# Kernel optimization log

Hardware: AMD Instinct MI355X
Metric: run time of the kernel (lower is better)

Reference implementation:

```python
import jax, jax.numpy as jnp
import numpy as np

B, N, C = 8, 1024, 768
H, D = 12, 64  # num_heads, head_dim; C == H*D
SCALE = 1.0 / np.sqrt(D)
NEG_INF = -1e9


def setup_inputs() -> dict:
    key = jax.random.key(0)
    k1, k2, k3, k4 = jax.random.split(key, 4)
    x = jax.random.normal(k1, (B, N, C), dtype=jnp.float32)
    # additive padding mask: 0 for valid tokens, -1e9 for padded tail
    lengths = jax.random.randint(k2, (B,), N // 2, N + 1)  # valid lengths per sample
    pad = jnp.arange(N)[None, :] >= lengths[:, None]       # [B, N] True = padded
    attn_mask = jnp.where(pad, NEG_INF, 0.0).astype(jnp.float32)[:, None, None, :]  # [B,1,1,N]
    W_qkv = jax.random.normal(k3, (C, 3 * C), dtype=jnp.float32) * (C ** -0.5)
    b_qkv = jnp.zeros((3 * C,), dtype=jnp.float32)
    W_proj = jax.random.normal(k4, (C, C), dtype=jnp.float32) * (C ** -0.5)
    b_proj = jnp.zeros((C,), dtype=jnp.float32)
    return {"x": x, "attn_mask": attn_mask, "W_qkv": W_qkv, "b_qkv": b_qkv,
            "W_proj": W_proj, "b_proj": b_proj}


def reference(x, attn_mask, W_qkv, b_qkv, W_proj, b_proj):
    qkv = (x @ W_qkv + b_qkv).reshape(B, N, 3, H, D)
    qkv = jnp.transpose(qkv, (2, 0, 3, 1, 4))
    q, k, v = qkv[0], qkv[1], qkv[2]
    attn = jnp.einsum('bhnd,bhmd->bhnm', q, k) * SCALE  # [B, H, N, N]
    attn = attn + attn_mask                              # broadcast [B,1,1,N]
    attn = jax.nn.softmax(attn, axis=-1)
    out = jnp.einsum('bhnm,bhmd->bhnd', attn, v)         # [B, H, N, D]
    out = jnp.transpose(out, (0, 2, 1, 3)).reshape(B, N, C)
    return out @ W_proj + b_proj
```

## Files before the change

kernel.cpp:

```cpp
#include <hip/hip_runtime.h>
#include <stdint.h>

#define NB 8
#define NHEAD 12
#define SEQ 1024
#define CDIM 768
#define HDIM 64

#define SCALE_L2E 0.1803368801111244f
#define L2E 1.4426950408889634f

typedef __attribute__((ext_vector_type(8))) short bf16x8;
typedef __attribute__((ext_vector_type(4))) short bf16x4;
typedef __attribute__((ext_vector_type(4))) float f32x4;
typedef __attribute__((ext_vector_type(4))) unsigned short us4;

__device__ __forceinline__ void gload_lds16(const void* g, void* l) {
  __builtin_amdgcn_global_load_lds((const __attribute__((address_space(1))) void*)g,
                                   (__attribute__((address_space(3))) void*)l,
                                   16, 0, 0);
}

__device__ __forceinline__ unsigned short f2bf(float f) {
  __bf16 h = (__bf16)f;
  return __builtin_bit_cast(unsigned short, h);
}

__device__ __forceinline__ f32x4 mfma16(bf16x8 a, bf16x8 b, f32x4 c) {
  return __builtin_amdgcn_mfma_f32_16x16x32_bf16(a, b, c, 0, 0, 0);
}


__global__ void cvt_x_kernel(const float* __restrict__ in,
                             unsigned short* __restrict__ out, int n8) {
  int i = blockIdx.x * blockDim.x + threadIdx.x;
  if (i >= n8) return;
  const float4* p = (const float4*)in;
  float4 a = p[2 * i], b = p[2 * i + 1];
  union { bf16x8 v; unsigned short h[8]; } u;
  u.h[0] = f2bf(a.x); u.h[1] = f2bf(a.y); u.h[2] = f2bf(a.z); u.h[3] = f2bf(a.w);
  u.h[4] = f2bf(b.x); u.h[5] = f2bf(b.y); u.h[6] = f2bf(b.z); u.h[7] = f2bf(b.w);
  ((bf16x8*)out)[i] = u.v;
}

__global__ void tconv_kernel(const float* __restrict__ in,
                             unsigned short* __restrict__ out, int K, int N) {
  __shared__ float tile[32][33];
  int tx = threadIdx.x & 31, ty = threadIdx.x >> 5;
  int n0 = blockIdx.x * 32, k0 = blockIdx.y * 32;
#pragma unroll
  for (int i = 0; i < 4; i++)
    tile[ty + 8 * i][tx] = in[(size_t)(k0 + ty + 8 * i) * N + n0 + tx];
  __syncthreads();
#pragma unroll
  for (int i = 0; i < 4; i++)
    out[(size_t)(n0 + ty + 8 * i) * K + k0 + tx] = f2bf(tile[tx][ty + 8 * i]);
}

template <int BM, int BN, int EPI>
__global__ __launch_bounds__(256, 4)
void gemm_bt_kernel(const unsigned short* __restrict__ A,
                    const unsigned short* __restrict__ Bt,
                    const float* __restrict__ bias,
                    unsigned short* __restrict__ q_out,
                    unsigned short* __restrict__ k_out,
                    unsigned short* __restrict__ v_out,
                    float* __restrict__ f_out,
                    int M, int N, int K) {
  constexpr int WM = BM / 2, WN = BN / 2;
  constexpr int MI = WM / 16, NJ = WN / 16;
  constexpr int CA = BM / 32, CB = BN / 32;
  __shared__ __align__(16) unsigned short As[BM * 64];
  __shared__ __align__(16) unsigned short Bs[BN * 64];
  const int t = threadIdx.x;
  const int w = t >> 6, l = t & 63;
  const int g = l >> 4, lr = l & 15;
  const int wr = w >> 1, wc = w & 1;
  const int nTN = N / BN;
  const int bpx = gridDim.x >> 3;
  const int orig = (blockIdx.x & 7) * bpx + (blockIdx.x >> 3);
  const int bm = orig / nTN, bn = orig % nTN;
  const int m0 = bm * BM, n0 = bn * BN;

  f32x4 acc[MI][NJ];
#pragma unroll
  for (int i = 0; i < MI; i++)
#pragma unroll
    for (int j = 0; j < NJ; j++) acc[i][j] = f32x4{0.f, 0.f, 0.f, 0.f};

  const unsigned short* aP[CA];
  const unsigned short* bP[CB];
#pragma unroll
  for (int i = 0; i < CA; i++) {
    int c = t + 256 * i, r = c >> 3, s = c & 7;
    aP[i] = A + (size_t)(m0 + r) * K + (s ^ (r & 7)) * 8;
  }
#pragma unroll
  for (int i = 0; i < CB; i++) {
    int c = t + 256 * i, r = c >> 3, s = c & 7;
    bP[i] = Bt + (size_t)(n0 + r) * K + (s ^ (r & 7)) * 8;
  }

  bf16x8 areg[CA], breg[CB];
  auto prefetch = [&](int kk) {
#pragma unroll
    for (int i = 0; i < CA; i++) areg[i] = *(const bf16x8*)(aP[i] + kk);
#pragma unroll
    for (int i = 0; i < CB; i++) breg[i] = *(const bf16x8*)(bP[i] + kk);
  };
  auto commit = [&]() {
#pragma unroll
    for (int i = 0; i < CA; i++) *(bf16x8*)(As + (t + 256 * i) * 8) = areg[i];
#pragma unroll
    for (int i = 0; i < CB; i++) *(bf16x8*)(Bs + (t + 256 * i) * 8) = breg[i];
  };

  prefetch(0);
  for (int kk = 0; kk < K; kk += 64) {
    commit();
    __syncthreads();
    if (kk + 64 < K) prefetch(kk + 64);
#pragma unroll
    for (int ks = 0; ks < 2; ks++) {
      const int slot = ((ks * 4 + g) ^ (lr & 7)) << 3;
      bf16x8 af[MI];
#pragma unroll
      for (int i = 0; i < MI; i++) {
        int row = wr * WM + i * 16 + lr;
        af[i] = *(const bf16x8*)(As + row * 64 + slot);
      }
#pragma unroll
      for (int j = 0; j < NJ; j++) {
        int row = wc * WN + j * 16 + lr;
        bf16x8 bfr = *(const bf16x8*)(Bs + row * 64 + slot);
#pragma unroll
        for (int i = 0; i < MI; i++) acc[i][j] = mfma16(af[i], bfr, acc[i][j]);
      }
    }
    __syncthreads();
  }

  float bv[NJ];
#pragma unroll
  for (int j = 0; j < NJ; j++) bv[j] = bias[n0 + wc * WN + j * 16 + lr];

  if (EPI == 1) {
#pragma unroll
    for (int i = 0; i < MI; i++) {
      int mrow = m0 + wr * WM + i * 16 + 4 * g;
#pragma unroll
      for (int j = 0; j < NJ; j++) {
        int n = n0 + wc * WN + j * 16 + lr;
#pragma unroll
        for (int r = 0; r < 4; r++)
          f_out[(size_t)(mrow + r) * N + n] = acc[i][j][r] + bv[j];
      }
    }
  } else {
    const int which = n0 / CDIM;
    const int bb = m0 / SEQ;
    const int tok0 = (m0 % SEQ) + wr * WM;
#pragma unroll
    for (int j = 0; j < NJ; j++) {
      int ncol = (n0 % CDIM) + wc * WN + j * 16;
      int hh = ncol / 64;
      int d = (ncol % 64) + lr;
#pragma unroll
      for (int i = 0; i < MI; i++) {
        int tokb = tok0 + i * 16 + 4 * g;
        if (which == 2) {
          us4 pk;
#pragma unroll
          for (int r = 0; r < 4; r++) pk[r] = f2bf(acc[i][j][r] + bv[j]);
          *(us4*)(v_out + ((size_t)(bb * NHEAD + hh) * 64 + d) * SEQ + tokb) = pk;
        } else {
          unsigned short* dst = (which == 0) ? q_out : k_out;
#pragma unroll
          for (int r = 0; r < 4; r++)
            dst[((size_t)(bb * NHEAD + hh) * SEQ + tokb + r) * 64 + d] =
                f2bf(acc[i][j][r] + bv[j]);
        }
      }
    }
  }
}

__global__ __launch_bounds__(256, 3)
void attn_kernel(const unsigned short* __restrict__ Qb,
                 const unsigned short* __restrict__ Kb,
                 const unsigned short* __restrict__ Vt,
                 const float* __restrict__ mask,
                 unsigned short* __restrict__ Ob) {
  __shared__ __align__(16) unsigned short Qs[128 * 64];
  __shared__ __align__(16) unsigned short Ks[128 * 64];
  __shared__ __align__(16) unsigned short Vs[64 * 128];
  __shared__ __align__(16) float smask[128];

  const int hwb = blockIdx.x;
  const int x = hwb & 7;
  const int i = hwb >> 3;
  const int qt = i & 7;
  const int bh = (i >> 3) * 8 + x;
  const int h = bh % NHEAD, b = bh / NHEAD;

  const int t = threadIdx.x, w = t >> 6, l = t & 63;
  const int g = l >> 4, lr = l & 15;

  const unsigned short* Qg = Qb + (((size_t)b * NHEAD + h) * SEQ + qt * 128) * 64;
  const unsigned short* Kg = Kb + ((size_t)b * NHEAD + h) * SEQ * 64;
  const unsigned short* Vg = Vt + ((size_t)b * NHEAD + h) * 64 * SEQ;
  const float* mg = mask + (size_t)b * SEQ;

  int nkb = 8;
#pragma unroll
  for (int kb = 7; kb >= 4; kb--)
    if (mg[kb * 128] < -1e8f) nkb = kb;

  bf16x8 kreg[4], vreg[4];
  float mreg;
  auto prefetch = [&](int kb) {
#pragma unroll
    for (int ii = 0; ii < 4; ii++) {
      int c = t + 256 * ii;
      int rk = c >> 3, sk = c & 7;
      kreg[ii] = *(const bf16x8*)(Kg + (size_t)(kb * 128 + rk) * 64 +
                                  ((sk ^ (rk & 7)) << 3));
      int rv = c >> 4, sv = c & 15;
      vreg[ii] = *(const bf16x8*)(Vg + (size_t)rv * SEQ + kb * 128 +
                                  ((sv ^ (rv & 7)) << 3));
    }
    mreg = (t < 128) ? mg[kb * 128 + t] * L2E : 0.f;
  };
  auto commit = [&]() {
#pragma unroll
    for (int ii = 0; ii < 4; ii++) {
      *(bf16x8*)(Ks + (t + 256 * ii) * 8) = kreg[ii];
      *(bf16x8*)(Vs + (t + 256 * ii) * 8) = vreg[ii];
    }
    if (t < 128) smask[t] = mreg;
  };

#pragma unroll
  for (int ii = 0; ii < 4; ii++) {
    int c = t + 256 * ii;
    int row = c >> 3, sl = c & 7;
    gload_lds16(Qg + row * 64 + ((sl ^ (row & 7)) << 3), Qs + c * 8);
  }
  prefetch(0);
  __syncthreads();

  bf16x8 qfr[2][2];
#pragma unroll
  for (int qi = 0; qi < 2; qi++)
#pragma unroll
    for (int ks = 0; ks < 2; ks++) {
      int row = w * 32 + qi * 16 + lr;
      qfr[qi][ks] =
          *(const bf16x8*)(Qs + row * 64 + (((ks * 4 + g) ^ (lr & 7)) << 3));
    }

  float l_run[2] = {0.f, 0.f};
  f32x4 oacc[2][4];
#pragma unroll
  for (int qi = 0; qi < 2; qi++)
#pragma unroll
    for (int df = 0; df < 4; df++) oacc[qi][df] = f32x4{0.f, 0.f, 0.f, 0.f};

  for (int kb = 0; kb < nkb; kb++) {
    __syncthreads();
    commit();
    __syncthreads();
    if (kb + 1 < nkb) prefetch(kb + 1);

    float bs[2] = {0.f, 0.f};
    bf16x8 pa[4][2];
#pragma unroll
    for (int kc = 0; kc < 4; kc++) {
      f32x4 s0[2], s1[2];
#pragma unroll
      for (int qi = 0; qi < 2; qi++) {
        s0[qi] = f32x4{0.f, 0.f, 0.f, 0.f};
        s1[qi] = f32x4{0.f, 0.f, 0.f, 0.f};
      }
#pragma unroll
      for (int ks = 0; ks < 2; ks++) {
        int row0 = (2 * kc) * 16 + lr;
        int row1 = (2 * kc + 1) * 16 + lr;
        int slot = ((ks * 4 + g) ^ (lr & 7)) << 3;
        bf16x8 a0 = *(const bf16x8*)(Ks + row0 * 64 + slot);
        bf16x8 a1 = *(const bf16x8*)(Ks + row1 * 64 + slot);
        s0[0] = mfma16(a0, qfr[0][ks], s0[0]);
        s0[1] = mfma16(a0, qfr[1][ks], s0[1]);
        s1[0] = mfma16(a1, qfr[0][ks], s1[0]);
        s1[1] = mfma16(a1, qfr[1][ks], s1[1]);
      }
      f32x4 mv0 = *(const f32x4*)(smask + (2 * kc) * 16 + 4 * g);
      f32x4 mv1 = *(const f32x4*)(smask + (2 * kc + 1) * 16 + 4 * g);
#pragma unroll
      for (int qi = 0; qi < 2; qi++) {
        union { bf16x8 v; unsigned short hh[8]; } u;
#pragma unroll
        for (int r = 0; r < 4; r++) {
          float p0 = __builtin_amdgcn_exp2f(fmaf(s0[qi][r], SCALE_L2E, mv0[r]));
          float p1 = __builtin_amdgcn_exp2f(fmaf(s1[qi][r], SCALE_L2E, mv1[r]));
          bs[qi] += p0 + p1;
          u.hh[r] = f2bf(p0);
          u.hh[4 + r] = f2bf(p1);
        }
        pa[kc][qi] = u.v;
      }
    }
    bs[0] += __shfl_xor(bs[0], 16);
    bs[0] += __shfl_xor(bs[0], 32);
    bs[1] += __shfl_xor(bs[1], 16);
    bs[1] += __shfl_xor(bs[1], 32);
    l_run[0] += bs[0];
    l_run[1] += bs[1];

    const int sw = (lr & 7) << 4;
#pragma unroll
    for (int kc = 0; kc < 4; kc++) {
#pragma unroll
      for (int df = 0; df < 4; df++) {
        const char* vp = (const char*)(Vs + (df * 16 + lr) * 128);
        bf16x4 lo = *(const bf16x4*)(vp + ((kc * 64 + 8 * g) ^ sw));
        bf16x4 hi = *(const bf16x4*)(vp + ((kc * 64 + 32 + 8 * g) ^ sw));
        bf16x8 vb = __builtin_shufflevector(lo, hi, 0, 1, 2, 3, 4, 5, 6, 7);
        oacc[0][df] = mfma16(pa[kc][0], vb, oacc[0][df]);
        oacc[1][df] = mfma16(pa[kc][1], vb, oacc[1][df]);
      }
    }
  }

#pragma unroll
  for (int qi = 0; qi < 2; qi++) {
    float linv = 1.f / l_run[qi];
#pragma unroll
    for (int r = 0; r < 4; r++) {
      float li = __shfl(linv, 4 * g + r);
      int tok = qt * 128 + w * 32 + qi * 16 + 4 * g + r;
#pragma unroll
      for (int df = 0; df < 4; df++) {
        float val = oacc[qi][df][r] * li;
        Ob[((size_t)b * SEQ + tok) * CDIM + h * 64 + df * 16 + lr] = f2bf(val);
      }
    }
  }
}

extern "C" void kernel_launch(void* const* d_in, const int* in_sizes, int n_in,
                              void* d_out, int out_size, void* d_ws,
                              size_t ws_size, hipStream_t stream) {
  const float* x = (const float*)d_in[0];
  const float* mask = (const float*)d_in[1];
  const float* Wqkv = (const float*)d_in[2];
  const float* bqkv = (const float*)d_in[3];
  const float* Wproj = (const float*)d_in[4];
  const float* bproj = (const float*)d_in[5];
  float* out = (float*)d_out;

  char* ws = (char*)d_ws;
  size_t off = 0;
  auto take = [&](size_t bytes) {
    char* p = ws + off;
    off += (bytes + 255) & ~(size_t)255;
    return p;
  };
  unsigned short* xb = (unsigned short*)take((size_t)NB * SEQ * CDIM * 2);
  unsigned short* wqt = (unsigned short*)take((size_t)3 * CDIM * CDIM * 2);
  unsigned short* wpt = (unsigned short*)take((size_t)CDIM * CDIM * 2);
  unsigned short* Qb = (unsigned short*)take((size_t)NB * NHEAD * SEQ * 64 * 2);
  unsigned short* Kbf = (unsigned short*)take((size_t)NB * NHEAD * SEQ * 64 * 2);
  unsigned short* Vt = (unsigned short*)take((size_t)NB * NHEAD * SEQ * 64 * 2);
  unsigned short* Ob = (unsigned short*)take((size_t)NB * SEQ * CDIM * 2);

  int n8 = NB * SEQ * CDIM / 8;
  cvt_x_kernel<<<(n8 + 255) / 256, 256, 0, stream>>>(x, xb, n8);
  tconv_kernel<<<dim3(3 * CDIM / 32, CDIM / 32), 256, 0, stream>>>(Wqkv, wqt,
                                                                   CDIM, 3 * CDIM);
  tconv_kernel<<<dim3(CDIM / 32, CDIM / 32), 256, 0, stream>>>(Wproj, wpt, CDIM,
                                                               CDIM);
  gemm_bt_kernel<128, 128, 0>
      <<<(NB * SEQ / 128) * (3 * CDIM / 128), 256, 0, stream>>>(
          xb, wqt, bqkv, Qb, Kbf, Vt, nullptr, NB * SEQ, 3 * CDIM, CDIM);
  attn_kernel<<<NB * NHEAD * 8, 256, 0, stream>>>(Qb, Kbf, Vt, mask, Ob);
  gemm_bt_kernel<64, 64, 1>
      <<<(NB * SEQ / 64) * (CDIM / 64), 256, 0, stream>>>(
          Ob, wpt, bproj, nullptr, nullptr, nullptr, out, NB * SEQ, CDIM, CDIM);
}
```

Measured before the change: 214.9 us.

## Double-buffer GEMM tiles via direct global-to-LDS loads and widen V swizzle

The GEMM main loop switches from register-staged prefetch to global_load_lds writes straight into double-buffered shared tiles. Explicit vmcnt waits and raw barriers let the next tile's load overlap the current tile's MFMAs. The attention kernel's V tile swizzle grows from 8 to 16 chunk positions to cut LDS bank conflicts on the split 8-byte V reads. Doubling shared memory lowers the occupancy hint to 2 for the QKV GEMM variant, which may reduce latency hiding.

```diff
diff --git a/kernel.cpp b/kernel.cpp
--- a/kernel.cpp
+++ b/kernel.cpp
@@ -28,6 +28,14 @@
 
 __device__ __forceinline__ f32x4 mfma16(bf16x8 a, bf16x8 b, f32x4 c) {
   return __builtin_amdgcn_mfma_f32_16x16x32_bf16(a, b, c, 0, 0, 0);
+}
+
+template <int N>
+__device__ __forceinline__ void s_waitcnt_vm() {
+  if constexpr (N == 0) asm volatile("s_waitcnt vmcnt(0)" ::: "memory");
+  else if constexpr (N == 4) asm volatile("s_waitcnt vmcnt(4)" ::: "memory");
+  else if constexpr (N == 8) asm volatile("s_waitcnt vmcnt(8)" ::: "memory");
+  else static_assert(N == 0, "unsupported vmcnt literal");
 }
 
 
@@ -58,7 +66,7 @@
 }
 
 template <int BM, int BN, int EPI>
-__global__ __launch_bounds__(256, 4)
+__global__ __launch_bounds__(256, EPI ? 4 : 2)
 void gemm_bt_kernel(const unsigned short* __restrict__ A,
                     const unsigned short* __restrict__ Bt,
                     const float* __restrict__ bias,
@@ -70,8 +78,9 @@
   constexpr int WM = BM / 2, WN = BN / 2;
   constexpr int MI = WM / 16, NJ = WN / 16;
   constexpr int CA = BM / 32, CB = BN / 32;
-  __shared__ __align__(16) unsigned short As[BM * 64];
-  __shared__ __align__(16) unsigned short Bs[BN * 64];
+  constexpr int LOADS = CA + CB;
+  __shared__ __align__(16) unsigned short As[2][BM * 64];
+  __shared__ __align__(16) unsigned short Bs[2][BN * 64];
   const int t = threadIdx.x;
   const int w = t >> 6, l = t & 63;
   const int g = l >> 4, lr = l & 15;
@@ -101,25 +110,29 @@
     bP[i] = Bt + (size_t)(n0 + r) * K + (s ^ (r & 7)) * 8;
   }
 
-  bf16x8 areg[CA], breg[CB];
-  auto prefetch = [&](int kk) {
-#pragma unroll
-    for (int i = 0; i < CA; i++) areg[i] = *(const bf16x8*)(aP[i] + kk);
-#pragma unroll
-    for (int i = 0; i < CB; i++) breg[i] = *(const bf16x8*)(bP[i] + kk);
+  auto stage = [&](int buf, int kk) {
+#pragma unroll
+    for (int i = 0; i < CA; i++)
+      gload_lds16(aP[i] + kk, As[buf] + (t + 256 * i) * 8);
+#pragma unroll
+    for (int i = 0; i < CB; i++)
+      gload_lds16(bP[i] + kk, Bs[buf] + (t + 256 * i) * 8);
   };
-  auto commit = [&]() {
-#pragma unroll
-    for (int i = 0; i < CA; i++) *(bf16x8*)(As + (t + 256 * i) * 8) = areg[i];
-#pragma unroll
-    for (int i = 0; i < CB; i++) *(bf16x8*)(Bs + (t + 256 * i) * 8) = breg[i];
-  };
-
-  prefetch(0);
-  for (int kk = 0; kk < K; kk += 64) {
-    commit();
-    __syncthreads();
-    if (kk + 64 < K) prefetch(kk + 64);
+
+  stage(0, 0);
+  const int nt = K >> 6;
+  for (int tt = 0; tt < nt; ++tt) {
+    const int cur = tt & 1;
+    if (tt + 1 < nt) {
+      stage(cur ^ 1, (tt + 1) << 6);
+      s_waitcnt_vm<LOADS>();
+    } else {
+      s_waitcnt_vm<0>();
+    }
+    __builtin_amdgcn_sched_barrier(0);
+    __builtin_amdgcn_s_barrier();
+    const unsigned short* Ab = As[cur];
+    const unsigned short* Bb = Bs[cur];
 #pragma unroll
     for (int ks = 0; ks < 2; ks++) {
       const int slot = ((ks * 4 + g) ^ (lr & 7)) << 3;
@@ -127,17 +140,19 @@
 #pragma unroll
       for (int i = 0; i < MI; i++) {
         int row = wr * WM + i * 16 + lr;
-        af[i] = *(const bf16x8*)(As + row * 64 + slot);
+        af[i] = *(const bf16x8*)(Ab + row * 64 + slot);
       }
 #pragma unroll
       for (int j = 0; j < NJ; j++) {
         int row = wc * WN + j * 16 + lr;
-        bf16x8 bfr = *(const bf16x8*)(Bs + row * 64 + slot);
+        bf16x8 bfr = *(const bf16x8*)(Bb + row * 64 + slot);
 #pragma unroll
         for (int i = 0; i < MI; i++) acc[i][j] = mfma16(af[i], bfr, acc[i][j]);
       }
     }
-    __syncthreads();
+    asm volatile("" ::: "memory");
+    __builtin_amdgcn_s_barrier();
+    __builtin_amdgcn_sched_barrier(0);
   }
 
   float bv[NJ];
@@ -227,7 +242,7 @@
                                   ((sk ^ (rk & 7)) << 3));
       int rv = c >> 4, sv = c & 15;
       vreg[ii] = *(const bf16x8*)(Vg + (size_t)rv * SEQ + kb * 128 +
-                                  ((sv ^ (rv & 7)) << 3));
+                                  ((sv ^ (rv & 15)) << 3));
     }
     mreg = (t < 128) ? mg[kb * 128 + t] * L2E : 0.f;
   };
@@ -317,14 +332,15 @@
     l_run[0] += bs[0];
     l_run[1] += bs[1];
 
-    const int sw = (lr & 7) << 4;
 #pragma unroll
     for (int kc = 0; kc < 4; kc++) {
+      const int c16lo = kc * 4 + (g >> 1);
+      const int odd = (g & 1) << 3;
 #pragma unroll
       for (int df = 0; df < 4; df++) {
         const char* vp = (const char*)(Vs + (df * 16 + lr) * 128);
-        bf16x4 lo = *(const bf16x4*)(vp + ((kc * 64 + 8 * g) ^ sw));
-        bf16x4 hi = *(const bf16x4*)(vp + ((kc * 64 + 32 + 8 * g) ^ sw));
+        bf16x4 lo = *(const bf16x4*)(vp + (((c16lo ^ lr) << 4) | odd));
+        bf16x4 hi = *(const bf16x4*)(vp + ((((c16lo + 2) ^ lr) << 4) | odd));
         bf16x8 vb = __builtin_shufflevector(lo, hi, 0, 1, 2, 3, 4, 5, 6, 7);
         oacc[0][df] = mfma16(pa[kc][0], vb, oacc[0][df]);
         oacc[1][df] = mfma16(pa[kc][1], vb, oacc[1][df]);
```

After: 203.3 us. -5.4%, faster.
